# Kernel tuning notes

Hardware: AMD Instinct MI355X
Metric: run time of the kernel (lower is better)

The kernel has to match this reference:

```python
import jax, jax.numpy as jnp
import numpy as np
from jax import lax

CHUNK = 256
ROPE_BASE = 10000.0


def setup_inputs() -> dict:
    D, H, K = 2048, 16, 4
    Dh = D // H
    key = jax.random.key(0)
    ks = jax.random.split(key, 8)
    x = jax.random.normal(ks[0], (2, 4096, D), dtype=jnp.float32)
    norm_scale = jnp.ones((D,), jnp.float32)
    conv_w = jax.random.normal(ks[1], (D, 1, K), jnp.float32) * 0.1
    conv_b = jnp.zeros((D,), jnp.float32)
    in_proj_w = jax.random.normal(ks[2], (3 * D, D), jnp.float32) * 0.02
    out_proj_w = jax.random.normal(ks[3], (D, D), jnp.float32) * 0.02
    # dt_bias init as in torch module
    u = jax.random.uniform(ks[4], (H, Dh), jnp.float32)
    dt = jnp.clip(jnp.exp(u * (np.log(0.1) - np.log(10.0)) + np.log(10.0)), 0.001, None)
    dt_bias = (dt + jnp.log(-jnp.expm1(-dt))).reshape(-1)
    head_mix = jnp.eye(H, dtype=jnp.float32)
    return {"x": x, "norm_scale": norm_scale, "conv_w": conv_w, "conv_b": conv_b,
            "in_proj_w": in_proj_w, "dt_bias": dt_bias, "head_mix": head_mix,
            "out_proj_w": out_proj_w}


def _forward(x, norm_scale, conv_w, conv_b, in_proj_w, dt_bias, head_mix, out_proj_w):
    B, N, D = x.shape
    H = head_mix.shape[0]
    Dh = D // H
    K = conv_w.shape[-1]
    residual = x
    # RMSNorm (fp32 with clamp)
    xf = x.astype(jnp.float32)
    rms = lax.rsqrt(jnp.mean(xf * xf, -1, keepdims=True) + 1e-6)
    xn = jnp.clip(norm_scale * xf * rms, -60000.0, 60000.0).astype(x.dtype)
    # causal depthwise conv1d (torch pads K-1 then truncates to N)
    xc = lax.conv_general_dilated(xn.transpose(0, 2, 1), conv_w, (1,), [(K - 1, 0)],
                                  dimension_numbers=("NCH", "OIH", "NCH"),
                                  feature_group_count=D)
    xc = xc + conv_b[None, :, None]
    xc = jax.nn.silu(xc.transpose(0, 2, 1))  # (B,N,D)
    fused = xc @ in_proj_w.T  # (B,N,3D)
    dt_raw, v, gate = jnp.split(fused, 3, axis=-1)
    dt = jnp.clip(jax.nn.softplus(dt_raw.astype(jnp.float32) + dt_bias), 0.001, 2.0)
    gate = jax.nn.sigmoid(gate)
    log_alpha = -dt  # (B,N,D) fp32
    # RoPE on v per head
    inv_freq = 1.0 / (ROPE_BASE ** (jnp.arange(0, Dh, 2, dtype=jnp.float32) / Dh))
    t = jnp.arange(N, dtype=jnp.float32)
    freqs = t[:, None] * inv_freq[None, :]  # (N, Dh//2)
    cos = jnp.cos(freqs)[None, :, None, :]
    sin = jnp.sin(freqs)[None, :, None, :]
    v4 = v.reshape(B, N, H, Dh)
    v1, v2 = v4[..., : Dh // 2], v4[..., Dh // 2:]
    v_rot = jnp.concatenate([v1 * cos - v2 * sin, v1 * sin + v2 * cos], -1).reshape(B, N, D)
    v_in = v_rot * dt  # fp32
    # pad to chunk multiple (static)
    pad = (-N) % CHUNK
    if pad:
        v_in = jnp.pad(v_in, ((0, 0), (0, pad), (0, 0)))
        log_alpha = jnp.pad(log_alpha, ((0, 0), (0, pad), (0, 0)))
    NC = v_in.shape[1] // CHUNK
    vc = v_in.reshape(B, NC, CHUNK, D)
    la = log_alpha.reshape(B, NC, CHUNK, D)
    # intra-chunk stabilized scan
    L = jnp.clip(jnp.cumsum(la, axis=2), -20.0, 0.0)
    Lmax = jnp.max(L, axis=2, keepdims=True)
    Ls = L - Lmax
    cum = jnp.cumsum(jnp.exp(-Ls) * vc, axis=2)
    chunk_out = jnp.exp(Ls) * cum
    if NC > 1:
        bd = L[:, :, -1, :]             # (B,NC,D) boundary decay
        bo = chunk_out[:, :, -1, :]     # boundary out
        cd = jnp.clip(jnp.cumsum(bd, axis=1), -80.0, 0.0)
        stab = jnp.max(cd, axis=1, keepdims=True)
        ncd = jnp.clip(cd - stab, -20.0, 0.0)
        seeds = bo * jnp.exp(-ncd)
        shifted = jnp.pad(seeds[:, :-1], ((0, 0), (1, 0), (0, 0)))
        carries = jnp.cumsum(shifted, axis=1) * jnp.exp(ncd)
        final = chunk_out + carries[:, :, None, :] * jnp.exp(L)
    else:
        final = chunk_out
    final = final.astype(x.dtype).reshape(B, -1, D)[:, :N, :]
    # head mixing
    vm = jnp.einsum("bnhd,hm->bnmd", final.reshape(B, N, H, Dh), head_mix).reshape(B, N, D)
    out = (vm * gate) @ out_proj_w.T
    return residual + out


def reference(x, norm_scale, conv_w, conv_b, in_proj_w, dt_bias, head_mix, out_proj_w):
    return _forward(x, norm_scale, conv_w, conv_b, in_proj_w, dt_bias, head_mix, out_proj_w)
```

## Files before the change

kernel.cpp:

```cpp
#include <hip/hip_runtime.h>
#include <hip/hip_bf16.h>
#include <math.h>

#define B_ 2
#define N_ 4096
#define D_ 2048
#define H_ 16
#define DH_ 128
#define CHUNK_ 256
#define NC_ 16
#define M_ (B_*N_)
#define F3D (3*D_)

typedef __bf16 v8bf __attribute__((ext_vector_type(8)));
typedef float  v4f  __attribute__((ext_vector_type(4)));
typedef unsigned short u16x8 __attribute__((ext_vector_type(8)));

__device__ __forceinline__ float bf2f(unsigned short u) {
    union { unsigned int i; float f; } c; c.i = ((unsigned int)u) << 16; return c.f;
}
__device__ __forceinline__ unsigned short f2bf(float f) {
    __hip_bfloat16 h = __float2bfloat16(f);
    return *(unsigned short*)&h;
}

__device__ __forceinline__ void async_copy16(void* lds, const void* g) {
    __builtin_amdgcn_global_load_lds(
        (const __attribute__((address_space(1))) unsigned int*)g,
        (__attribute__((address_space(3))) unsigned int*)lds,
        16, 0, 0);
}

__global__ __launch_bounds__(256) void k_rmsnorm(const float* __restrict__ x,
                                                 const float* __restrict__ scale,
                                                 __hip_bfloat16* __restrict__ xn)
{
    __shared__ float red[4];
    const int row = blockIdx.x;
    const float4* x4 = (const float4*)(x + (size_t)row * D_);
    float4 a = x4[threadIdx.x*2];
    float4 b = x4[threadIdx.x*2 + 1];
    float ss = a.x*a.x + a.y*a.y + a.z*a.z + a.w*a.w
             + b.x*b.x + b.y*b.y + b.z*b.z + b.w*b.w;
    #pragma unroll
    for (int off = 32; off > 0; off >>= 1) ss += __shfl_down(ss, off, 64);
    if ((threadIdx.x & 63) == 0) red[threadIdx.x >> 6] = ss;
    __syncthreads();
    float tot = red[0] + red[1] + red[2] + red[3];
    float r = rsqrtf(tot / (float)D_ + 1e-6f);
    const float4* s4 = (const float4*)scale;
    float4 sa = s4[threadIdx.x*2];
    float4 sb = s4[threadIdx.x*2 + 1];
    float v[8] = { sa.x*a.x, sa.y*a.y, sa.z*a.z, sa.w*a.w,
                   sb.x*b.x, sb.y*b.y, sb.z*b.z, sb.w*b.w };
    u16x8 o;
    #pragma unroll
    for (int j = 0; j < 8; ++j) {
        float t = fminf(fmaxf(v[j]*r, -60000.f), 60000.f);
        o[j] = f2bf(t);
    }
    ((u16x8*)(xn + (size_t)row * D_))[threadIdx.x] = o;
}

__global__ __launch_bounds__(256) void k_conv_silu(const __hip_bfloat16* __restrict__ xn,
                                                   const float* __restrict__ w,
                                                   const float* __restrict__ bias,
                                                   __hip_bfloat16* __restrict__ xc)
{
    size_t p = (size_t)blockIdx.x * 256 + threadIdx.x;
    size_t e0 = p * 8;
    int d0 = (int)(e0 & (D_-1));
    int n  = (int)((e0 >> 11) & (N_-1));
    const float4* w4 = (const float4*)w;
    float acc[8];
    const float4* b4 = (const float4*)(bias + d0);
    float4 ba = b4[0], bb = b4[1];
    acc[0]=ba.x; acc[1]=ba.y; acc[2]=ba.z; acc[3]=ba.w;
    acc[4]=bb.x; acc[5]=bb.y; acc[6]=bb.z; acc[7]=bb.w;
    float4 wv[8];
    #pragma unroll
    for (int j = 0; j < 8; ++j) wv[j] = w4[d0 + j];
    #pragma unroll
    for (int k = 0; k < 4; ++k) {
        int nn = n - 3 + k;
        if (nn >= 0) {
            u16x8 t = *(const u16x8*)(xn + e0 - (size_t)(3-k)*D_);
            #pragma unroll
            for (int j = 0; j < 8; ++j) {
                float wk = (k==0)?wv[j].x:(k==1)?wv[j].y:(k==2)?wv[j].z:wv[j].w;
                acc[j] += bf2f(t[j]) * wk;
            }
        }
    }
    u16x8 o;
    #pragma unroll
    for (int j = 0; j < 8; ++j) {
        float s = acc[j] / (1.f + __expf(-acc[j]));
        o[j] = f2bf(s);
    }
    *(u16x8*)(xc + e0) = o;
}

#define W1_VECS 1572864
__global__ __launch_bounds__(256) void k_cast2(const float* __restrict__ s1,
                                               __hip_bfloat16* __restrict__ d1,
                                               const float* __restrict__ s2,
                                               __hip_bfloat16* __restrict__ d2)
{
    size_t p = (size_t)blockIdx.x * 256 + threadIdx.x;
    const float* src; __hip_bfloat16* dst; size_t q;
    if (p < W1_VECS) { src = s1; dst = d1; q = p; }
    else             { src = s2; dst = d2; q = p - W1_VECS; }
    const float4* s4 = (const float4*)src;
    float4 a = s4[q*2], b = s4[q*2 + 1];
    u16x8 o;
    o[0]=f2bf(a.x); o[1]=f2bf(a.y); o[2]=f2bf(a.z); o[3]=f2bf(a.w);
    o[4]=f2bf(b.x); o[5]=f2bf(b.y); o[6]=f2bf(b.z); o[7]=f2bf(b.w);
    ((u16x8*)dst)[q] = o;
}

template<int MODE>
__global__ __launch_bounds__(256, 4) void k_gemm(const __hip_bfloat16* __restrict__ Abf,
                                              const __hip_bfloat16* __restrict__ Wbf,
                                              __hip_bfloat16* __restrict__ o0,
                                              __hip_bfloat16* __restrict__ o1,
                                              __hip_bfloat16* __restrict__ o2,
                                              const float* __restrict__ dt_bias,
                                              const float* __restrict__ resid,
                                              float* __restrict__ outp)
{
    __shared__ __attribute__((aligned(16))) char lds[2][2][8192];
    const __bf16* A = (const __bf16*)Abf;
    const __bf16* W = (const __bf16*)Wbf;
    const int tid  = threadIdx.x;
    const int wave = tid >> 6;
    const int lane = tid & 63;
    const size_t m0 = (size_t)blockIdx.x * 128;
    const size_t n0 = (size_t)blockIdx.y * 128;
    const int wm = (wave & 1) * 64;
    const int wn = (wave >> 1) * 64;

    v4f acc[4][4] = {};

    const int fr = lane & 15;
    const int qk = lane >> 4;
    int mA = wm + fr, rA = mA >> 1;
    int mB = wn + fr, rB = mB >> 1;
    const char* vA = &lds[0][0][0] + rA*128 + (((((mA&1)<<2)|qk) ^ (rA&7)) << 4);
    const char* vB = &lds[0][1][0] + rB*128 + (((((mB&1)<<2)|qk) ^ (rB&7)) << 4);

    const int srL = lane >> 3, ssL = lane & 7;
    const __bf16 *sA0, *sA1, *sB0, *sB1;
    {
        int r0 = wave*8 + srL,      u0 = ssL ^ (r0 & 7);
        int r1 = 32 + wave*8 + srL, u1 = ssL ^ (r1 & 7);
        int ma0 = 2*r0 + (u0 >> 2), kg0 = u0 & 3;
        int ma1 = 2*r1 + (u1 >> 2), kg1 = u1 & 3;
        sA0 = A + (m0 + ma0)*(size_t)2048 + kg0*8;
        sA1 = A + (m0 + ma1)*(size_t)2048 + kg1*8;
        sB0 = W + (n0 + ma0)*(size_t)2048 + kg0*8;
        sB1 = W + (n0 + ma1)*(size_t)2048 + kg1*8;
    }
    char* dA0 = &lds[0][0][0] + wave*1024;
    char* dB0 = &lds[0][1][0] + wave*1024;

    #define STAGE(BUF) do { \
        async_copy16(dA0 + (BUF)*16384,        sA0); \
        async_copy16(dA0 + (BUF)*16384 + 4096, sA1); \
        async_copy16(dB0 + (BUF)*16384,        sB0); \
        async_copy16(dB0 + (BUF)*16384 + 4096, sB1); \
        sA0 += 32; sA1 += 32; sB0 += 32; sB1 += 32; } while(0)

    STAGE(0);

    for (int i2 = 0; i2 < 32; ++i2) {
        asm volatile("s_waitcnt vmcnt(0)" ::: "memory");
        __builtin_amdgcn_s_barrier();
        __builtin_amdgcn_sched_barrier(0);
        STAGE(1);
        {
            v8bf fa[4], fb[4];
            #pragma unroll
            for (int i = 0; i < 4; ++i) fa[i] = *(const v8bf*)(vA + i*1024);
            #pragma unroll
            for (int j = 0; j < 4; ++j) fb[j] = *(const v8bf*)(vB + j*1024);
            __builtin_amdgcn_s_setprio(1);
            #pragma unroll
            for (int i = 0; i < 4; ++i)
                #pragma unroll
                for (int j = 0; j < 4; ++j)
                    acc[i][j] = __builtin_amdgcn_mfma_f32_16x16x32_bf16(fa[i], fb[j], acc[i][j], 0, 0, 0);
            __builtin_amdgcn_s_setprio(0);
        }
        asm volatile("s_waitcnt vmcnt(0)" ::: "memory");
        __builtin_amdgcn_s_barrier();
        __builtin_amdgcn_sched_barrier(0);
        if (i2 + 1 < 32) STAGE(0);
        {
            v8bf fa[4], fb[4];
            #pragma unroll
            for (int i = 0; i < 4; ++i) fa[i] = *(const v8bf*)(vA + 16384 + i*1024);
            #pragma unroll
            for (int j = 0; j < 4; ++j) fb[j] = *(const v8bf*)(vB + 16384 + j*1024);
            __builtin_amdgcn_s_setprio(1);
            #pragma unroll
            for (int i = 0; i < 4; ++i)
                #pragma unroll
                for (int j = 0; j < 4; ++j)
                    acc[i][j] = __builtin_amdgcn_mfma_f32_16x16x32_bf16(fa[i], fb[j], acc[i][j], 0, 0, 0);
            __builtin_amdgcn_s_setprio(0);
        }
    }
    #undef STAGE

    const int col = lane & 15;
    const int rb  = (lane >> 4) * 4;
    if (MODE == 0) {
        const int stream = blockIdx.y >> 4;
        const size_t nb = n0 - (size_t)stream * D_;
        #pragma unroll
        for (int i = 0; i < 4; ++i)
            #pragma unroll
            for (int j = 0; j < 4; ++j) {
                size_t nIdx = nb + wn + j*16 + col;
                #pragma unroll
                for (int r = 0; r < 4; ++r) {
                    size_t m = m0 + wm + i*16 + rb + r;
                    size_t off = m * (size_t)D_ + nIdx;
                    float v = acc[i][j][r];
                    if (stream == 0) {
                        float xx = v + dt_bias[nIdx];
                        float e  = __expf(-fabsf(xx));
                        float sp = fmaxf(xx, 0.f) + __logf(1.f + e);
                        float dt = fminf(fmaxf(sp, 0.001f), 2.0f);
                        o0[off] = __float2bfloat16(-dt);
                    } else if (stream == 1) {
                        o1[off] = __float2bfloat16(v);
                    } else {
                        o2[off] = __float2bfloat16(1.f/(1.f+__expf(-v)));
                    }
                }
            }
    } else {
        #pragma unroll
        for (int i = 0; i < 4; ++i)
            #pragma unroll
            for (int j = 0; j < 4; ++j)
                #pragma unroll
                for (int r = 0; r < 4; ++r) {
                    size_t m = m0 + wm + i*16 + rb + r;
                    size_t off = m * (size_t)D_ + n0 + wn + j*16 + col;
                    outp[off] = acc[i][j][r] + resid[off];
                }
    }
}

__global__ __launch_bounds__(256) void k_scan1(const __hip_bfloat16* __restrict__ la,
                                               const __hip_bfloat16* __restrict__ v,
                                               float* __restrict__ bd, float* __restrict__ bo,
                                               float* __restrict__ nc,
                                               __hip_bfloat16* __restrict__ expL)
{
    int idx = blockIdx.x * 256 + threadIdx.x;
    int d = idx & (D_-1);
    int c = (idx >> 11) & (NC_-1);
    int b = idx >> 15;
    int i = d & 63;
    const bool firstHalf = (d & 64) == 0;
    float inv = __expf((float)i * (-9.210340371976184f / 64.f));
    int n0 = c * CHUNK_;
    float cs = cosf((float)n0 * inv), sn = sinf((float)n0 * inv);
    float ca = cosf(inv), sa = sinf(inv);
    size_t row0 = (size_t)b * N_ + (size_t)c * CHUNK_;
    float S = 0.f, Lp = 0.f, out = 0.f;
    #pragma unroll 8
    for (int t = 0; t < CHUNK_; ++t) {
        size_t off = (row0 + t) * (size_t)D_ + d;
        float a  = __bfloat162float(la[off]);
        float vo = __bfloat162float(v[off]);
        float vp = __bfloat162float(v[firstHalf ? off + 64 : off - 64]);
        float dt = -a;
        float vin = (firstHalf ? (vo*cs - vp*sn) : (vp*sn + vo*cs)) * dt;
        S += a;
        float L = fmaxf(S, -20.f);
        out = __expf(L - Lp) * out + vin;
        Lp = L;
        nc[off]   = out;
        expL[off] = __float2bfloat16(__expf(L));
        float csn = cs*ca - sn*sa;
        sn = sn*ca + cs*sa;
        cs = csn;
    }
    bd[idx] = Lp;
    bo[idx] = out;
}

__global__ __launch_bounds__(256) void k_scan2(const float* __restrict__ bd,
                                               const float* __restrict__ bo,
                                               float* __restrict__ carries)
{
    int idx = blockIdx.x * 256 + threadIdx.x;
    int d = idx & (D_-1);
    int b = idx >> 11;
    float bd0 = bd[(size_t)(b*NC_)*D_ + d];
    float cd = 0.f, acc = 0.f;
    #pragma unroll
    for (int c = 0; c < NC_; ++c) {
        size_t o = (size_t)(b*NC_ + c)*D_ + d;
        cd = fmaxf(cd + bd[o], -80.f);
        float ncd = fmaxf(cd - bd0, -20.f);
        carries[o] = acc * __expf(ncd);
        acc += bo[o] * __expf(-ncd);
    }
}

__global__ __launch_bounds__(256) void k_hmix(const float* __restrict__ nc,
                                              const __hip_bfloat16* __restrict__ expL,
                                              const float* __restrict__ carr,
                                              const __hip_bfloat16* __restrict__ gate,
                                              const float* __restrict__ hm,
                                              __hip_bfloat16* __restrict__ y)
{
    __shared__ float lf[D_];
    __shared__ float lhm[H_*H_];
    const int row = blockIdx.x;
    const size_t base = (size_t)row * D_;
    const int b = row >> 12;
    const int c = (row >> 8) & (NC_-1);
    const float* cp = carr + ((size_t)(b*NC_ + c)) * D_ + threadIdx.x*8;
    u16x8 el = ((const u16x8*)(expL + base))[threadIdx.x];
    const float4* n4 = (const float4*)(nc + base + threadIdx.x*8);
    float4 na = n4[0], nb = n4[1];
    const float4* c4 = (const float4*)cp;
    float4 ca = c4[0], cb = c4[1];
    float nv[8] = { na.x, na.y, na.z, na.w, nb.x, nb.y, nb.z, nb.w };
    float cv[8] = { ca.x, ca.y, ca.z, ca.w, cb.x, cb.y, cb.z, cb.w };
    #pragma unroll
    for (int j = 0; j < 8; ++j)
        lf[threadIdx.x*8 + j] = nv[j] + cv[j] * bf2f(el[j]);
    lhm[threadIdx.x] = hm[threadIdx.x];
    __syncthreads();
    #pragma unroll
    for (int k = 0; k < 8; ++k) {
        int o = threadIdx.x + k*256;
        int m  = o >> 7;
        int dh = o & 127;
        float s = 0.f;
        #pragma unroll
        for (int h = 0; h < H_; ++h) s += lf[h*DH_ + dh] * lhm[h*H_ + m];
        float g = __bfloat162float(gate[base + o]);
        y[base + o] = __float2bfloat16(s * g);
    }
}

extern "C" void kernel_launch(void* const* d_in, const int* in_sizes, int n_in,
                              void* d_out, int out_size, void* d_ws, size_t ws_size,
                              hipStream_t stream)
{
    const float* x          = (const float*)d_in[0];
    const float* norm_scale = (const float*)d_in[1];
    const float* conv_w     = (const float*)d_in[2];
    const float* conv_b     = (const float*)d_in[3];
    const float* in_proj_w  = (const float*)d_in[4];
    const float* dt_bias    = (const float*)d_in[5];
    const float* head_mix   = (const float*)d_in[6];
    const float* out_proj_w = (const float*)d_in[7];
    float* out = (float*)d_out;

    char* ws = (char*)d_ws;
    __hip_bfloat16* la   = (__hip_bfloat16*)ws;
    __hip_bfloat16* xn   = (__hip_bfloat16*)(ws + 67108864);
    __hip_bfloat16* xc   = (__hip_bfloat16*)(ws + 100663296);
    __hip_bfloat16* gate = (__hip_bfloat16*)(ws + 134217728);
    __hip_bfloat16* w2   = (__hip_bfloat16*)(ws + 167772160);
    float*          bd   = (float*)(ws + 176160768);
    float*          bo   = (float*)(ws + 176422912);
    float*          carr = (float*)(ws + 176685056);
    __hip_bfloat16* w1   = xn;
    float*          nc   = (float*)(ws + 67108864);
    __hip_bfloat16* y    = (__hip_bfloat16*)ws;
    __hip_bfloat16* v     = (__hip_bfloat16*)d_out;
    __hip_bfloat16* stex  = (__hip_bfloat16*)((char*)d_out + 33554432);

    k_rmsnorm<<<M_, 256, 0, stream>>>(x, norm_scale, xn);
    k_conv_silu<<<(M_*(size_t)D_)/8/256, 256, 0, stream>>>(xn, conv_w, conv_b, xc);
    k_cast2<<<8192, 256, 0, stream>>>(in_proj_w, w1, out_proj_w, w2);
    k_gemm<0><<<dim3(M_/128, F3D/128), 256, 0, stream>>>(xc, w1, la, v, gate, dt_bias, nullptr, nullptr);
    k_scan1<<<(B_*NC_*D_)/256, 256, 0, stream>>>(la, v, bd, bo, nc, stex);
    k_scan2<<<(B_*D_)/256, 256, 0, stream>>>(bd, bo, carr);
    k_hmix<<<M_, 256, 0, stream>>>(nc, stex, carr, gate, head_mix, y);
    k_gemm<1><<<dim3(M_/128, D_/128), 256, 0, stream>>>(y, w2, nullptr, nullptr, nullptr, nullptr, x, out);
}
```

Before: 637.1 us.

## Split scan chunks into half-chunks, store nc in bf16, fuse conv and cast kernels

The intra-chunk scan now uses two threads per channel and chunk. Each thread covers a 128-step half: it first pre-sums the decay over the first half, then scans its own half. This doubles parallelism in the latency-bound scan. The cross-chunk pass now combines the half-chunk boundaries and emits per-half carries. The intermediate nc buffer is stored in bf16 instead of fp32 to halve its traffic, at some precision cost. The conv/SiLU and weight-cast kernels are merged into one launch.

```diff
diff --git a/kernel.cpp b/kernel.cpp
--- a/kernel.cpp
+++ b/kernel.cpp
@@ -62,61 +62,61 @@
     ((u16x8*)(xn + (size_t)row * D_))[threadIdx.x] = o;
 }
 
-__global__ __launch_bounds__(256) void k_conv_silu(const __hip_bfloat16* __restrict__ xn,
-                                                   const float* __restrict__ w,
-                                                   const float* __restrict__ bias,
-                                                   __hip_bfloat16* __restrict__ xc)
-{
-    size_t p = (size_t)blockIdx.x * 256 + threadIdx.x;
-    size_t e0 = p * 8;
-    int d0 = (int)(e0 & (D_-1));
-    int n  = (int)((e0 >> 11) & (N_-1));
-    const float4* w4 = (const float4*)w;
-    float acc[8];
-    const float4* b4 = (const float4*)(bias + d0);
-    float4 ba = b4[0], bb = b4[1];
-    acc[0]=ba.x; acc[1]=ba.y; acc[2]=ba.z; acc[3]=ba.w;
-    acc[4]=bb.x; acc[5]=bb.y; acc[6]=bb.z; acc[7]=bb.w;
-    float4 wv[8];
-    #pragma unroll
-    for (int j = 0; j < 8; ++j) wv[j] = w4[d0 + j];
-    #pragma unroll
-    for (int k = 0; k < 4; ++k) {
-        int nn = n - 3 + k;
-        if (nn >= 0) {
-            u16x8 t = *(const u16x8*)(xn + e0 - (size_t)(3-k)*D_);
-            #pragma unroll
-            for (int j = 0; j < 8; ++j) {
-                float wk = (k==0)?wv[j].x:(k==1)?wv[j].y:(k==2)?wv[j].z:wv[j].w;
-                acc[j] += bf2f(t[j]) * wk;
+#define W1_VECS 1572864
+__global__ __launch_bounds__(256) void k_prep(const __hip_bfloat16* __restrict__ xn,
+                                              const float* __restrict__ w,
+                                              const float* __restrict__ bias,
+                                              __hip_bfloat16* __restrict__ xc,
+                                              const float* __restrict__ s1,
+                                              __hip_bfloat16* __restrict__ d1,
+                                              const float* __restrict__ s2,
+                                              __hip_bfloat16* __restrict__ d2)
+{
+    if (blockIdx.x < 8192) {
+        size_t p = (size_t)blockIdx.x * 256 + threadIdx.x;
+        size_t e0 = p * 8;
+        int d0 = (int)(e0 & (D_-1));
+        int n  = (int)((e0 >> 11) & (N_-1));
+        const float4* w4 = (const float4*)w;
+        float acc[8];
+        const float4* b4 = (const float4*)(bias + d0);
+        float4 ba = b4[0], bb = b4[1];
+        acc[0]=ba.x; acc[1]=ba.y; acc[2]=ba.z; acc[3]=ba.w;
+        acc[4]=bb.x; acc[5]=bb.y; acc[6]=bb.z; acc[7]=bb.w;
+        float4 wv[8];
+        #pragma unroll
+        for (int j = 0; j < 8; ++j) wv[j] = w4[d0 + j];
+        #pragma unroll
+        for (int k = 0; k < 4; ++k) {
+            int nn = n - 3 + k;
+            if (nn >= 0) {
+                u16x8 t = *(const u16x8*)(xn + e0 - (size_t)(3-k)*D_);
+                #pragma unroll
+                for (int j = 0; j < 8; ++j) {
+                    float wk = (k==0)?wv[j].x:(k==1)?wv[j].y:(k==2)?wv[j].z:wv[j].w;
+                    acc[j] += bf2f(t[j]) * wk;
+                }
             }
         }
-    }
-    u16x8 o;
-    #pragma unroll
-    for (int j = 0; j < 8; ++j) {
-        float s = acc[j] / (1.f + __expf(-acc[j]));
-        o[j] = f2bf(s);
-    }
-    *(u16x8*)(xc + e0) = o;
-}
-
-#define W1_VECS 1572864
-__global__ __launch_bounds__(256) void k_cast2(const float* __restrict__ s1,
-                                               __hip_bfloat16* __restrict__ d1,
-                                               const float* __restrict__ s2,
-                                               __hip_bfloat16* __restrict__ d2)
-{
-    size_t p = (size_t)blockIdx.x * 256 + threadIdx.x;
-    const float* src; __hip_bfloat16* dst; size_t q;
-    if (p < W1_VECS) { src = s1; dst = d1; q = p; }
-    else             { src = s2; dst = d2; q = p - W1_VECS; }
-    const float4* s4 = (const float4*)src;
-    float4 a = s4[q*2], b = s4[q*2 + 1];
-    u16x8 o;
-    o[0]=f2bf(a.x); o[1]=f2bf(a.y); o[2]=f2bf(a.z); o[3]=f2bf(a.w);
-    o[4]=f2bf(b.x); o[5]=f2bf(b.y); o[6]=f2bf(b.z); o[7]=f2bf(b.w);
-    ((u16x8*)dst)[q] = o;
+        u16x8 o;
+        #pragma unroll
+        for (int j = 0; j < 8; ++j) {
+            float s = acc[j] / (1.f + __expf(-acc[j]));
+            o[j] = f2bf(s);
+        }
+        *(u16x8*)(xc + e0) = o;
+    } else {
+        size_t p = (size_t)(blockIdx.x - 8192) * 256 + threadIdx.x;
+        const float* src; __hip_bfloat16* dst; size_t q;
+        if (p < W1_VECS) { src = s1; dst = d1; q = p; }
+        else             { src = s2; dst = d2; q = p - W1_VECS; }
+        const float4* s4 = (const float4*)src;
+        float4 a = s4[q*2], b = s4[q*2 + 1];
+        u16x8 o;
+        o[0]=f2bf(a.x); o[1]=f2bf(a.y); o[2]=f2bf(a.z); o[3]=f2bf(a.w);
+        o[4]=f2bf(b.x); o[5]=f2bf(b.y); o[6]=f2bf(b.z); o[7]=f2bf(b.w);
+        ((u16x8*)dst)[q] = o;
+    }
 }
 
 template<int MODE>
@@ -257,66 +257,84 @@
 
 __global__ __launch_bounds__(256) void k_scan1(const __hip_bfloat16* __restrict__ la,
                                                const __hip_bfloat16* __restrict__ v,
-                                               float* __restrict__ bd, float* __restrict__ bo,
-                                               float* __restrict__ nc,
+                                               float* __restrict__ bdH, float* __restrict__ boH,
+                                               __hip_bfloat16* __restrict__ nc,
                                                __hip_bfloat16* __restrict__ expL)
 {
-    int idx = blockIdx.x * 256 + threadIdx.x;
-    int d = idx & (D_-1);
-    int c = (idx >> 11) & (NC_-1);
-    int b = idx >> 15;
+    __shared__ float hsum[256];
+    const int lanePair = threadIdx.x & 127;
+    const int half = threadIdx.x >> 7;
+    int pairIdx = blockIdx.x * 128 + lanePair;
+    int d = pairIdx & (D_-1);
+    int c = (pairIdx >> 11) & (NC_-1);
+    int b = pairIdx >> 15;
+    size_t rowH = (size_t)b * N_ + (size_t)c * CHUNK_ + half*128;
+
+    float S0 = 0.f;
+    #pragma unroll 8
+    for (int t = 0; t < 128; ++t)
+        S0 += __bfloat162float(la[(rowH + t) * (size_t)D_ + d]);
+    hsum[threadIdx.x] = S0;
+    __syncthreads();
+    float S = half ? hsum[lanePair] : 0.f;
+
     int i = d & 63;
-    const bool firstHalf = (d & 64) == 0;
+    const bool fh = (d & 64) == 0;
     float inv = __expf((float)i * (-9.210340371976184f / 64.f));
-    int n0 = c * CHUNK_;
+    int n0 = c * CHUNK_ + half * 128;
     float cs = cosf((float)n0 * inv), sn = sinf((float)n0 * inv);
     float ca = cosf(inv), sa = sinf(inv);
-    size_t row0 = (size_t)b * N_ + (size_t)c * CHUNK_;
-    float S = 0.f, Lp = 0.f, out = 0.f;
+    float Lp = 0.f, out = 0.f;
     #pragma unroll 8
-    for (int t = 0; t < CHUNK_; ++t) {
-        size_t off = (row0 + t) * (size_t)D_ + d;
+    for (int t = 0; t < 128; ++t) {
+        size_t off = (rowH + t) * (size_t)D_ + d;
         float a  = __bfloat162float(la[off]);
         float vo = __bfloat162float(v[off]);
-        float vp = __bfloat162float(v[firstHalf ? off + 64 : off - 64]);
+        float vp = __bfloat162float(v[fh ? off + 64 : off - 64]);
         float dt = -a;
-        float vin = (firstHalf ? (vo*cs - vp*sn) : (vp*sn + vo*cs)) * dt;
+        float vin = (fh ? (vo*cs - vp*sn) : (vp*sn + vo*cs)) * dt;
         S += a;
         float L = fmaxf(S, -20.f);
         out = __expf(L - Lp) * out + vin;
         Lp = L;
-        nc[off]   = out;
+        nc[off]   = __float2bfloat16(out);
         expL[off] = __float2bfloat16(__expf(L));
         float csn = cs*ca - sn*sa;
         sn = sn*ca + cs*sa;
         cs = csn;
     }
-    bd[idx] = Lp;
-    bo[idx] = out;
-}
-
-__global__ __launch_bounds__(256) void k_scan2(const float* __restrict__ bd,
-                                               const float* __restrict__ bo,
-                                               float* __restrict__ carries)
+    size_t hIdx = ((size_t)(b*NC_ + c)*2 + half)*D_ + d;
+    bdH[hIdx] = Lp;
+    boH[hIdx] = out;
+}
+
+__global__ __launch_bounds__(256) void k_scan2(const float* __restrict__ bdH,
+                                               const float* __restrict__ boH,
+                                               float* __restrict__ carrH)
 {
     int idx = blockIdx.x * 256 + threadIdx.x;
     int d = idx & (D_-1);
     int b = idx >> 11;
-    float bd0 = bd[(size_t)(b*NC_)*D_ + d];
+    auto HIX = [&](int c, int h) { return ((size_t)(b*NC_ + c)*2 + h)*D_ + d; };
+    float bd0 = bdH[HIX(0,1)];
     float cd = 0.f, acc = 0.f;
     #pragma unroll
     for (int c = 0; c < NC_; ++c) {
-        size_t o = (size_t)(b*NC_ + c)*D_ + d;
-        cd = fmaxf(cd + bd[o], -80.f);
+        float bdA = bdH[HIX(c,0)], boA = boH[HIX(c,0)];
+        float bdB = bdH[HIX(c,1)], boB = boH[HIX(c,1)];
+        float bo_c = boB + boA * __expf(bdB - bdA);
+        cd = fmaxf(cd + bdB, -80.f);
         float ncd = fmaxf(cd - bd0, -20.f);
-        carries[o] = acc * __expf(ncd);
-        acc += bo[o] * __expf(-ncd);
-    }
-}
-
-__global__ __launch_bounds__(256) void k_hmix(const float* __restrict__ nc,
+        float carr = acc * __expf(ncd);
+        carrH[HIX(c,0)] = carr;
+        carrH[HIX(c,1)] = carr + boA * __expf(-bdA);
+        acc += bo_c * __expf(-ncd);
+    }
+}
+
+__global__ __launch_bounds__(256) void k_hmix(const __hip_bfloat16* __restrict__ nc,
                                               const __hip_bfloat16* __restrict__ expL,
-                                              const float* __restrict__ carr,
+                                              const float* __restrict__ carrH,
                                               const __hip_bfloat16* __restrict__ gate,
                                               const float* __restrict__ hm,
                                               __hip_bfloat16* __restrict__ y)
@@ -325,19 +343,18 @@
     __shared__ float lhm[H_*H_];
     const int row = blockIdx.x;
     const size_t base = (size_t)row * D_;
-    const int b = row >> 12;
-    const int c = (row >> 8) & (NC_-1);
-    const float* cp = carr + ((size_t)(b*NC_ + c)) * D_ + threadIdx.x*8;
+    const int b  = row >> 12;
+    const int c  = (row >> 8) & (NC_-1);
+    const int hf = (row >> 7) & 1;
+    const float* cp = carrH + ((size_t)(b*NC_ + c)*2 + hf) * D_ + threadIdx.x*8;
     u16x8 el = ((const u16x8*)(expL + base))[threadIdx.x];
-    const float4* n4 = (const float4*)(nc + base + threadIdx.x*8);
-    float4 na = n4[0], nb = n4[1];
+    u16x8 n8 = ((const u16x8*)(nc + base))[threadIdx.x];
     const float4* c4 = (const float4*)cp;
     float4 ca = c4[0], cb = c4[1];
-    float nv[8] = { na.x, na.y, na.z, na.w, nb.x, nb.y, nb.z, nb.w };
     float cv[8] = { ca.x, ca.y, ca.z, ca.w, cb.x, cb.y, cb.z, cb.w };
     #pragma unroll
     for (int j = 0; j < 8; ++j)
-        lf[threadIdx.x*8 + j] = nv[j] + cv[j] * bf2f(el[j]);
+        lf[threadIdx.x*8 + j] = bf2f(n8[j]) + cv[j] * bf2f(el[j]);
     lhm[threadIdx.x] = hm[threadIdx.x];
     __syncthreads();
     #pragma unroll
@@ -369,25 +386,25 @@
 
     char* ws = (char*)d_ws;
     __hip_bfloat16* la   = (__hip_bfloat16*)ws;
+    float*          bdH  = (float*)(ws + 33554432);
+    float*          boH  = (float*)(ws + 34078720);
+    float*          carrH= (float*)(ws + 34603008);
     __hip_bfloat16* xn   = (__hip_bfloat16*)(ws + 67108864);
     __hip_bfloat16* xc   = (__hip_bfloat16*)(ws + 100663296);
     __hip_bfloat16* gate = (__hip_bfloat16*)(ws + 134217728);
     __hip_bfloat16* w2   = (__hip_bfloat16*)(ws + 167772160);
-    float*          bd   = (float*)(ws + 176160768);
-    float*          bo   = (float*)(ws + 176422912);
-    float*          carr = (float*)(ws + 176685056);
     __hip_bfloat16* w1   = xn;
-    float*          nc   = (float*)(ws + 67108864);
+    __hip_bfloat16* nc   = (__hip_bfloat16*)(ws + 67108864);
     __hip_bfloat16* y    = (__hip_bfloat16*)ws;
     __hip_bfloat16* v     = (__hip_bfloat16*)d_out;
     __hip_bfloat16* stex  = (__hip_bfloat16*)((char*)d_out + 33554432);
 
     k_rmsnorm<<<M_, 256, 0, stream>>>(x, norm_scale, xn);
-    k_conv_silu<<<(M_*(size_t)D_)/8/256, 256, 0, stream>>>(xn, conv_w, conv_b, xc);
-    k_cast2<<<8192, 256, 0, stream>>>(in_proj_w, w1, out_proj_w, w2);
+    k_prep<<<16384, 256, 0, stream>>>(xn, conv_w, conv_b, xc,
+                                      in_proj_w, w1, out_proj_w, w2);
     k_gemm<0><<<dim3(M_/128, F3D/128), 256, 0, stream>>>(xc, w1, la, v, gate, dt_bias, nullptr, nullptr);
-    k_scan1<<<(B_*NC_*D_)/256, 256, 0, stream>>>(la, v, bd, bo, nc, stex);
-    k_scan2<<<(B_*D_)/256, 256, 0, stream>>>(bd, bo, carr);
-    k_hmix<<<M_, 256, 0, stream>>>(nc, stex, carr, gate, head_mix, y);
+    k_scan1<<<(B_*NC_*D_*2)/256, 256, 0, stream>>>(la, v, bdH, boH, nc, stex);
+    k_scan2<<<(B_*D_)/256, 256, 0, stream>>>(bdH, boH, carrH);
+    k_hmix<<<M_, 256, 0, stream>>>(nc, stex, carrH, gate, head_mix, y);
     k_gemm<1><<<dim3(M_/128, D_/128), 256, 0, stream>>>(y, w2, nullptr, nullptr, nullptr, nullptr, x, out);
 }
```

Result: no change. 644.8 us (+1.2%).

## Fuse RMSNorm, conv+SiLU and weight cast; store scan output as bf16

Applied to the files above, without the earlier changes.

Merges the RMSNorm, causal depthwise conv+SiLU and weight-cast kernels into one launch. Each row block recomputes the norms of its three preceding rows, so the bf16 normalized intermediate is never written or read back, at the cost of reading x four times and computing four reductions per block. The intra-chunk scan output is also stored as bf16 instead of fp32, halving that buffer's traffic into the head-mix kernel. This adds rounding error on the scan values, and the normalized input is no longer rounded to bf16 before the conv.

```diff
diff --git a/kernel.cpp b/kernel.cpp
--- a/kernel.cpp
+++ b/kernel.cpp
@@ -31,92 +31,90 @@
         16, 0, 0);
 }
 
-__global__ __launch_bounds__(256) void k_rmsnorm(const float* __restrict__ x,
-                                                 const float* __restrict__ scale,
-                                                 __hip_bfloat16* __restrict__ xn)
-{
-    __shared__ float red[4];
-    const int row = blockIdx.x;
-    const float4* x4 = (const float4*)(x + (size_t)row * D_);
-    float4 a = x4[threadIdx.x*2];
-    float4 b = x4[threadIdx.x*2 + 1];
-    float ss = a.x*a.x + a.y*a.y + a.z*a.z + a.w*a.w
-             + b.x*b.x + b.y*b.y + b.z*b.z + b.w*b.w;
-    #pragma unroll
-    for (int off = 32; off > 0; off >>= 1) ss += __shfl_down(ss, off, 64);
-    if ((threadIdx.x & 63) == 0) red[threadIdx.x >> 6] = ss;
-    __syncthreads();
-    float tot = red[0] + red[1] + red[2] + red[3];
-    float r = rsqrtf(tot / (float)D_ + 1e-6f);
-    const float4* s4 = (const float4*)scale;
-    float4 sa = s4[threadIdx.x*2];
-    float4 sb = s4[threadIdx.x*2 + 1];
-    float v[8] = { sa.x*a.x, sa.y*a.y, sa.z*a.z, sa.w*a.w,
-                   sb.x*b.x, sb.y*b.y, sb.z*b.z, sb.w*b.w };
-    u16x8 o;
-    #pragma unroll
-    for (int j = 0; j < 8; ++j) {
-        float t = fminf(fmaxf(v[j]*r, -60000.f), 60000.f);
-        o[j] = f2bf(t);
-    }
-    ((u16x8*)(xn + (size_t)row * D_))[threadIdx.x] = o;
-}
-
-__global__ __launch_bounds__(256) void k_conv_silu(const __hip_bfloat16* __restrict__ xn,
-                                                   const float* __restrict__ w,
-                                                   const float* __restrict__ bias,
-                                                   __hip_bfloat16* __restrict__ xc)
-{
-    size_t p = (size_t)blockIdx.x * 256 + threadIdx.x;
-    size_t e0 = p * 8;
-    int d0 = (int)(e0 & (D_-1));
-    int n  = (int)((e0 >> 11) & (N_-1));
-    const float4* w4 = (const float4*)w;
-    float acc[8];
-    const float4* b4 = (const float4*)(bias + d0);
-    float4 ba = b4[0], bb = b4[1];
-    acc[0]=ba.x; acc[1]=ba.y; acc[2]=ba.z; acc[3]=ba.w;
-    acc[4]=bb.x; acc[5]=bb.y; acc[6]=bb.z; acc[7]=bb.w;
-    float4 wv[8];
-    #pragma unroll
-    for (int j = 0; j < 8; ++j) wv[j] = w4[d0 + j];
-    #pragma unroll
-    for (int k = 0; k < 4; ++k) {
-        int nn = n - 3 + k;
-        if (nn >= 0) {
-            u16x8 t = *(const u16x8*)(xn + e0 - (size_t)(3-k)*D_);
-            #pragma unroll
-            for (int j = 0; j < 8; ++j) {
-                float wk = (k==0)?wv[j].x:(k==1)?wv[j].y:(k==2)?wv[j].z:wv[j].w;
-                acc[j] += bf2f(t[j]) * wk;
+#define W1_VECS 1572864
+__global__ __launch_bounds__(256) void k_prep(const float* __restrict__ x,
+                                              const float* __restrict__ scale,
+                                              const float* __restrict__ w,
+                                              const float* __restrict__ bias,
+                                              __hip_bfloat16* __restrict__ xc,
+                                              const float* __restrict__ s1,
+                                              __hip_bfloat16* __restrict__ d1,
+                                              const float* __restrict__ s2,
+                                              __hip_bfloat16* __restrict__ d2)
+{
+    if (blockIdx.x < 8192) {
+        __shared__ float red[4][4];
+        const int tid = threadIdx.x;
+        const int row = blockIdx.x;
+        const int pos = row & (N_-1);
+        float xr[4][8];
+        float ssv[4];
+        #pragma unroll
+        for (int k = 0; k < 4; ++k) {
+            if (pos - 3 + k >= 0) {
+                const float4* x4 = (const float4*)(x + (size_t)(row - 3 + k) * D_);
+                float4 a = x4[tid*2], b = x4[tid*2 + 1];
+                xr[k][0]=a.x; xr[k][1]=a.y; xr[k][2]=a.z; xr[k][3]=a.w;
+                xr[k][4]=b.x; xr[k][5]=b.y; xr[k][6]=b.z; xr[k][7]=b.w;
+                ssv[k] = a.x*a.x + a.y*a.y + a.z*a.z + a.w*a.w
+                       + b.x*b.x + b.y*b.y + b.z*b.z + b.w*b.w;
+            } else {
+                #pragma unroll
+                for (int j = 0; j < 8; ++j) xr[k][j] = 0.f;
+                ssv[k] = 0.f;
             }
         }
-    }
-    u16x8 o;
-    #pragma unroll
-    for (int j = 0; j < 8; ++j) {
-        float s = acc[j] / (1.f + __expf(-acc[j]));
-        o[j] = f2bf(s);
-    }
-    *(u16x8*)(xc + e0) = o;
-}
-
-#define W1_VECS 1572864
-__global__ __launch_bounds__(256) void k_cast2(const float* __restrict__ s1,
-                                               __hip_bfloat16* __restrict__ d1,
-                                               const float* __restrict__ s2,
-                                               __hip_bfloat16* __restrict__ d2)
-{
-    size_t p = (size_t)blockIdx.x * 256 + threadIdx.x;
-    const float* src; __hip_bfloat16* dst; size_t q;
-    if (p < W1_VECS) { src = s1; dst = d1; q = p; }
-    else             { src = s2; dst = d2; q = p - W1_VECS; }
-    const float4* s4 = (const float4*)src;
-    float4 a = s4[q*2], b = s4[q*2 + 1];
-    u16x8 o;
-    o[0]=f2bf(a.x); o[1]=f2bf(a.y); o[2]=f2bf(a.z); o[3]=f2bf(a.w);
-    o[4]=f2bf(b.x); o[5]=f2bf(b.y); o[6]=f2bf(b.z); o[7]=f2bf(b.w);
-    ((u16x8*)dst)[q] = o;
+        #pragma unroll
+        for (int off = 32; off > 0; off >>= 1)
+            #pragma unroll
+            for (int k = 0; k < 4; ++k) ssv[k] += __shfl_down(ssv[k], off, 64);
+        if ((tid & 63) == 0)
+            #pragma unroll
+            for (int k = 0; k < 4; ++k) red[k][tid >> 6] = ssv[k];
+        __syncthreads();
+        float rr[4];
+        #pragma unroll
+        for (int k = 0; k < 4; ++k)
+            rr[k] = rsqrtf((red[k][0]+red[k][1]+red[k][2]+red[k][3]) / (float)D_ + 1e-6f);
+
+        const int d0 = tid * 8;
+        const float4* s4 = (const float4*)(scale + d0);
+        float4 sa = s4[0], sb = s4[1];
+        float sc[8] = { sa.x, sa.y, sa.z, sa.w, sb.x, sb.y, sb.z, sb.w };
+        const float4* w4 = (const float4*)w;
+        float acc[8];
+        const float4* b4 = (const float4*)(bias + d0);
+        float4 ba = b4[0], bb = b4[1];
+        acc[0]=ba.x; acc[1]=ba.y; acc[2]=ba.z; acc[3]=ba.w;
+        acc[4]=bb.x; acc[5]=bb.y; acc[6]=bb.z; acc[7]=bb.w;
+        #pragma unroll
+        for (int j = 0; j < 8; ++j) {
+            float4 wv = w4[d0 + j];
+            float xn0 = fminf(fmaxf(sc[j]*xr[0][j]*rr[0], -60000.f), 60000.f);
+            float xn1 = fminf(fmaxf(sc[j]*xr[1][j]*rr[1], -60000.f), 60000.f);
+            float xn2 = fminf(fmaxf(sc[j]*xr[2][j]*rr[2], -60000.f), 60000.f);
+            float xn3 = fminf(fmaxf(sc[j]*xr[3][j]*rr[3], -60000.f), 60000.f);
+            acc[j] += xn0*wv.x + xn1*wv.y + xn2*wv.z + xn3*wv.w;
+        }
+        u16x8 o;
+        #pragma unroll
+        for (int j = 0; j < 8; ++j) {
+            float s = acc[j] / (1.f + __expf(-acc[j]));
+            o[j] = f2bf(s);
+        }
+        ((u16x8*)(xc + (size_t)row * D_))[tid] = o;
+    } else {
+        size_t p = (size_t)(blockIdx.x - 8192) * 256 + threadIdx.x;
+        const float* src; __hip_bfloat16* dst; size_t q;
+        if (p < W1_VECS) { src = s1; dst = d1; q = p; }
+        else             { src = s2; dst = d2; q = p - W1_VECS; }
+        const float4* s4 = (const float4*)src;
+        float4 a = s4[q*2], b = s4[q*2 + 1];
+        u16x8 o;
+        o[0]=f2bf(a.x); o[1]=f2bf(a.y); o[2]=f2bf(a.z); o[3]=f2bf(a.w);
+        o[4]=f2bf(b.x); o[5]=f2bf(b.y); o[6]=f2bf(b.z); o[7]=f2bf(b.w);
+        ((u16x8*)dst)[q] = o;
+    }
 }
 
 template<int MODE>
@@ -258,7 +256,7 @@
 __global__ __launch_bounds__(256) void k_scan1(const __hip_bfloat16* __restrict__ la,
                                                const __hip_bfloat16* __restrict__ v,
                                                float* __restrict__ bd, float* __restrict__ bo,
-                                               float* __restrict__ nc,
+                                               __hip_bfloat16* __restrict__ nc,
                                                __hip_bfloat16* __restrict__ expL)
 {
     int idx = blockIdx.x * 256 + threadIdx.x;
@@ -266,7 +264,7 @@
     int c = (idx >> 11) & (NC_-1);
     int b = idx >> 15;
     int i = d & 63;
-    const bool firstHalf = (d & 64) == 0;
+    const bool fh = (d & 64) == 0;
     float inv = __expf((float)i * (-9.210340371976184f / 64.f));
     int n0 = c * CHUNK_;
     float cs = cosf((float)n0 * inv), sn = sinf((float)n0 * inv);
@@ -278,14 +276,14 @@
         size_t off = (row0 + t) * (size_t)D_ + d;
         float a  = __bfloat162float(la[off]);
         float vo = __bfloat162float(v[off]);
-        float vp = __bfloat162float(v[firstHalf ? off + 64 : off - 64]);
+        float vp = __bfloat162float(v[fh ? off + 64 : off - 64]);
         float dt = -a;
-        float vin = (firstHalf ? (vo*cs - vp*sn) : (vp*sn + vo*cs)) * dt;
+        float vin = (fh ? (vo*cs - vp*sn) : (vp*sn + vo*cs)) * dt;
         S += a;
         float L = fmaxf(S, -20.f);
         out = __expf(L - Lp) * out + vin;
         Lp = L;
-        nc[off]   = out;
+        nc[off]   = __float2bfloat16(out);
         expL[off] = __float2bfloat16(__expf(L));
         float csn = cs*ca - sn*sa;
         sn = sn*ca + cs*sa;
@@ -314,7 +312,7 @@
     }
 }
 
-__global__ __launch_bounds__(256) void k_hmix(const float* __restrict__ nc,
+__global__ __launch_bounds__(256) void k_hmix(const __hip_bfloat16* __restrict__ nc,
                                               const __hip_bfloat16* __restrict__ expL,
                                               const float* __restrict__ carr,
                                               const __hip_bfloat16* __restrict__ gate,
@@ -329,15 +327,13 @@
     const int c = (row >> 8) & (NC_-1);
     const float* cp = carr + ((size_t)(b*NC_ + c)) * D_ + threadIdx.x*8;
     u16x8 el = ((const u16x8*)(expL + base))[threadIdx.x];
-    const float4* n4 = (const float4*)(nc + base + threadIdx.x*8);
-    float4 na = n4[0], nb = n4[1];
+    u16x8 n8 = ((const u16x8*)(nc + base))[threadIdx.x];
     const float4* c4 = (const float4*)cp;
     float4 ca = c4[0], cb = c4[1];
-    float nv[8] = { na.x, na.y, na.z, na.w, nb.x, nb.y, nb.z, nb.w };
     float cv[8] = { ca.x, ca.y, ca.z, ca.w, cb.x, cb.y, cb.z, cb.w };
     #pragma unroll
     for (int j = 0; j < 8; ++j)
-        lf[threadIdx.x*8 + j] = nv[j] + cv[j] * bf2f(el[j]);
+        lf[threadIdx.x*8 + j] = bf2f(n8[j]) + cv[j] * bf2f(el[j]);
     lhm[threadIdx.x] = hm[threadIdx.x];
     __syncthreads();
     #pragma unroll
@@ -369,22 +365,20 @@
 
     char* ws = (char*)d_ws;
     __hip_bfloat16* la   = (__hip_bfloat16*)ws;
-    __hip_bfloat16* xn   = (__hip_bfloat16*)(ws + 67108864);
+    float*          bd   = (float*)(ws + 33554432);
+    float*          bo   = (float*)(ws + 33816576);
+    float*          carr = (float*)(ws + 34078720);
+    __hip_bfloat16* w1   = (__hip_bfloat16*)(ws + 67108864);
     __hip_bfloat16* xc   = (__hip_bfloat16*)(ws + 100663296);
     __hip_bfloat16* gate = (__hip_bfloat16*)(ws + 134217728);
     __hip_bfloat16* w2   = (__hip_bfloat16*)(ws + 167772160);
-    float*          bd   = (float*)(ws + 176160768);
-    float*          bo   = (float*)(ws + 176422912);
-    float*          carr = (float*)(ws + 176685056);
-    __hip_bfloat16* w1   = xn;
-    float*          nc   = (float*)(ws + 67108864);
+    __hip_bfloat16* nc   = (__hip_bfloat16*)(ws + 67108864);
     __hip_bfloat16* y    = (__hip_bfloat16*)ws;
     __hip_bfloat16* v     = (__hip_bfloat16*)d_out;
     __hip_bfloat16* stex  = (__hip_bfloat16*)((char*)d_out + 33554432);
 
-    k_rmsnorm<<<M_, 256, 0, stream>>>(x, norm_scale, xn);
-    k_conv_silu<<<(M_*(size_t)D_)/8/256, 256, 0, stream>>>(xn, conv_w, conv_b, xc);
-    k_cast2<<<8192, 256, 0, stream>>>(in_proj_w, w1, out_proj_w, w2);
+    k_prep<<<16384, 256, 0, stream>>>(x, norm_scale, conv_w, conv_b, xc,
+                                      in_proj_w, w1, out_proj_w, w2);
     k_gemm<0><<<dim3(M_/128, F3D/128), 256, 0, stream>>>(xc, w1, la, v, gate, dt_bias, nullptr, nullptr);
     k_scan1<<<(B_*NC_*D_)/256, 256, 0, stream>>>(la, v, bd, bo, nc, stex);
     k_scan2<<<(B_*D_)/256, 256, 0, stream>>>(bd, bo, carr);
```

Result: no change. 647.1 us (+1.6%).
